# Performance work log

Measured on AMD Instinct MI355X. Metric: run time of the kernel, lower is better.

## Reference

```python
import jax, jax.numpy as jnp
import numpy as np

N_HEADS = 16
ROPE_BASE = 10000.0


def setup_inputs() -> dict:
    key = jax.random.key(0)
    k1, k2, k3 = jax.random.split(key, 3)
    B, L, D = 2, 2048, 2048
    x = jax.random.normal(k1, (B, L, D), dtype=jnp.float32)
    w_qkv = jax.random.normal(k2, (D, 3 * D), dtype=jnp.float32) * (1.0 / np.sqrt(D))
    w_out = jax.random.normal(k3, (D, D), dtype=jnp.float32) * (1.0 / np.sqrt(D))
    return {"x": x, "w_qkv": w_qkv, "w_out": w_out}


def _rope_cos_sin(L, head_dim, dtype):
    # inv_freq over even dims, freqs duplicated across both halves (HF convention)
    inv_freq = 1.0 / (ROPE_BASE ** (jnp.arange(0, head_dim, 2, dtype=jnp.float32) / head_dim))
    freqs = jnp.arange(L, dtype=jnp.float32)[:, None] * inv_freq[None, :]  # [L, hd/2]
    emb = jnp.concatenate([freqs, freqs], axis=-1)  # [L, hd]
    return jnp.cos(emb).astype(dtype), jnp.sin(emb).astype(dtype)


def _rotate_half(t):
    h = t.shape[-1] // 2
    return jnp.concatenate([-t[..., h:], t[..., :h]], axis=-1)


def reference(x, w_qkv, w_out):
    B, L, D = x.shape
    H = N_HEADS
    hd = D // H
    qkv = x @ w_qkv  # [B, L, 3D]
    q, k, v = jnp.split(qkv, 3, axis=-1)

    def heads(t):  # [B, L, D] -> [B, H, L, hd]
        return t.reshape(B, L, H, hd).transpose(0, 2, 1, 3)

    q, k, v = heads(q), heads(k), heads(v)
    cos, sin = _rope_cos_sin(L, hd, x.dtype)  # [L, hd] broadcast over B,H
    q = q * cos + _rotate_half(q) * sin
    k = k * cos + _rotate_half(k) * sin
    # SDPA, no mask, no dropout (eval), not causal
    scale = 1.0 / np.sqrt(hd)
    scores = jnp.einsum('bhld,bhsd->bhls', q, k) * scale
    attn = jax.nn.softmax(scores, axis=-1)
    y = jnp.einsum('bhls,bhsd->bhld', attn, v)  # [B, H, L, hd]
    y = y.transpose(0, 2, 1, 3).reshape(B, L, D)
    return y @ w_out
```

## Files before the change

kernel.cpp:

```cpp
#include <hip/hip_runtime.h>

typedef __attribute__((ext_vector_type(8))) short bf16x8;
typedef __attribute__((ext_vector_type(8))) unsigned short u16x8;
typedef __attribute__((ext_vector_type(4))) float f32x4;
typedef __attribute__((ext_vector_type(16))) float f32x16;
typedef __attribute__((ext_vector_type(4))) unsigned short u16x4;
typedef __attribute__((ext_vector_type(4))) unsigned int u32x4;
typedef unsigned int u32;

#define BB 2
#define LL 2048
#define DD 2048
#define HH 16
#define HDIM 128
#define MM 4096
#define NQKV 6144

__device__ __forceinline__ unsigned short f2bf(float f) {
    unsigned int u = __builtin_bit_cast(unsigned int, f);
    u += 0x7FFFu + ((u >> 16) & 1u);
    return (unsigned short)(u >> 16);
}
__device__ __forceinline__ float bf2f(unsigned short h) {
    unsigned int u = ((unsigned int)h) << 16;
    return __builtin_bit_cast(float, u);
}

__device__ __forceinline__ void gload16(const unsigned short* g, unsigned short* l) {
    __builtin_amdgcn_global_load_lds((const __attribute__((address_space(1))) void*)g,
                                     (__attribute__((address_space(3))) void*)l, 16, 0, 0);
}

__device__ __forceinline__ u32 cvtpk(float lo, float hi) {
    u32 r;
    asm("v_cvt_pk_bf16_f32 %0, %1, %2" : "=v"(r) : "v"(lo), "v"(hi));
    return r;
}
__device__ __forceinline__ void plswap(u32& a, u32& b) {
    asm("v_permlane32_swap_b32 %0, %1" : "+v"(a), "+v"(b));
}

__global__ __launch_bounds__(256) void k_prep(const float* __restrict__ x, unsigned short* __restrict__ xb,
                                              const float* __restrict__ wqkv, unsigned short* __restrict__ wqkvT,
                                              const float* __restrict__ wout, unsigned short* __restrict__ woutT,
                                              float* __restrict__ ct, float* __restrict__ st) {
    __shared__ unsigned short t[64][72];
    int bid = blockIdx.x;
    int tid = threadIdx.x;
    if (bid < 8192) {
        int i = bid * 256 + tid;
        float4 v = reinterpret_cast<const float4*>(x)[i];
        u16x4 o;
        o[0] = f2bf(v.x); o[1] = f2bf(v.y); o[2] = f2bf(v.z); o[3] = f2bf(v.w);
        reinterpret_cast<u16x4*>(xb)[i] = o;
        return;
    }
    if (bid >= 12288) {
        int idx = (bid - 12288) * 256 + tid;
        int pos = idx >> 6, d = idx & 63;
        float freq = __expf(-(float)d * (9.210340371976184f / 64.0f));
        float ang = (float)pos * freq;
        ct[idx] = cosf(ang);
        st[idx] = sinf(ang);
        return;
    }
    const float* in; unsigned short* out; int K, N, n0, k0;
    if (bid < 11264) {
        int r = bid - 8192;
        in = wqkv; out = wqkvT; K = DD; N = NQKV;
        n0 = (r % 96) * 64; k0 = (r / 96) * 64;
    } else {
        int r = bid - 11264;
        in = wout; out = woutT; K = DD; N = DD;
        n0 = (r & 31) * 64; k0 = (r >> 5) * 64;
    }
    int tr = tid >> 4, tc = tid & 15;
    #pragma unroll
    for (int i = 0; i < 4; ++i) {
        int k = i * 16 + tr;
        float4 v = *reinterpret_cast<const float4*>(in + (size_t)(k0 + k) * N + n0 + tc * 4);
        t[tc * 4 + 0][k] = f2bf(v.x);
        t[tc * 4 + 1][k] = f2bf(v.y);
        t[tc * 4 + 2][k] = f2bf(v.z);
        t[tc * 4 + 3][k] = f2bf(v.w);
    }
    __syncthreads();
    #pragma unroll
    for (int i = 0; i < 4; ++i) {
        int n = i * 16 + tr;
        u16x4 o = *reinterpret_cast<u16x4*>(&t[n][tc * 4]);
        *reinterpret_cast<u16x4*>(out + (size_t)(n0 + n) * K + k0 + tc * 4) = o;
    }
}

__global__ __launch_bounds__(256) void k_transV(const unsigned short* __restrict__ in,
                                                unsigned short* __restrict__ out) {
    __shared__ unsigned short t[64][68];
    int l0 = blockIdx.x * 64, d0 = blockIdx.y * 64;
    int bh = blockIdx.z;
    const unsigned short* ib = in + (size_t)bh * LL * HDIM;
    unsigned short* ob = out + (size_t)bh * HDIM * LL;
    int tid = threadIdx.x;
    int tr = tid >> 4, tc = tid & 15;
    #pragma unroll
    for (int i = 0; i < 4; ++i) {
        int l = i * 16 + tr;
        u16x4 v = *reinterpret_cast<const u16x4*>(ib + (size_t)(l0 + l) * HDIM + d0 + tc * 4);
        t[tc * 4 + 0][l] = v[0];
        t[tc * 4 + 1][l] = v[1];
        t[tc * 4 + 2][l] = v[2];
        t[tc * 4 + 3][l] = v[3];
    }
    __syncthreads();
    #pragma unroll
    for (int i = 0; i < 4; ++i) {
        int d = i * 16 + tr;
        u16x4 o = *reinterpret_cast<u16x4*>(&t[d][tc * 4]);
        *reinterpret_cast<u16x4*>(ob + (size_t)(d0 + d) * LL + l0 + tc * 4) = o;
    }
}

__global__ __launch_bounds__(256) void k_rope_apply(unsigned short* __restrict__ Q,
                                                    unsigned short* __restrict__ K,
                                                    const float* __restrict__ ct,
                                                    const float* __restrict__ st) {
    int idx = blockIdx.x * 256 + threadIdx.x;
    int d = idx & 63;
    int pos = (idx >> 6) & (LL - 1);
    int bh = idx >> 17;
    size_t base = ((size_t)bh * LL + pos) * HDIM;
    float c = ct[pos * 64 + d], s = st[pos * 64 + d];
    float q0 = bf2f(Q[base + d]), q1 = bf2f(Q[base + d + 64]);
    Q[base + d]      = f2bf(q0 * c - q1 * s);
    Q[base + d + 64] = f2bf(q1 * c + q0 * s);
    float k0 = bf2f(K[base + d]), k1 = bf2f(K[base + d + 64]);
    K[base + d]      = f2bf(k0 * c - k1 * s);
    K[base + d + 64] = f2bf(k1 * c + k0 * s);
}

__global__ __launch_bounds__(512, 2) void k_gemm384(const unsigned short* __restrict__ A,
                                                    const unsigned short* __restrict__ Bt,
                                                    unsigned short* __restrict__ outQ,
                                                    unsigned short* __restrict__ outK,
                                                    unsigned short* __restrict__ outV) {
    __shared__ unsigned short sm[3 * 20480];
    const int Kn = DD;
    const int tid = threadIdx.x;
    const int lane = tid & 63, w = tid >> 6;
    const int wm = w >> 2, wn = w & 3;
    const int lrow = lane & 15, lgrp = lane >> 4;
    const int NT = Kn / 32;

    int orig = blockIdx.x;
    int tau = (orig & 7) * 32 + (orig >> 3);
    const int m0 = (tau & 15) * 256, n0 = (tau >> 4) * 384;

    const int srow = lane >> 2, scol = lane & 3;
    const int scolg = ((scol ^ ((srow >> 1) & 3)) * 8);
    const int fcol  = ((lgrp ^ ((lrow >> 1) & 3)) * 8);

    f32x4 acc[8][6] = {};

    auto stageA = [&](int t, int r) {
        unsigned short* dst = sm + (t % 3) * 20480 + (r * 128 + w * 16) * 32;
        gload16(A + (size_t)(m0 + r * 128 + w * 16 + srow) * Kn + t * 32 + scolg, dst);
    };
    auto stageB = [&](int t, int r) {
        unsigned short* dst = sm + (t % 3) * 20480 + 8192 + (r * 128 + w * 16) * 32;
        gload16(Bt + (size_t)(n0 + r * 128 + w * 16 + srow) * Kn + t * 32 + scolg, dst);
    };

    auto body = [&](int t, bool doStage) {
        unsigned short* bufA = sm + (t % 3) * 20480;
        unsigned short* bufB = bufA + 8192;
        bf16x8 af[8], bfr[2];
        #pragma unroll
        for (int f = 0; f < 8; ++f)
            af[f] = *reinterpret_cast<const bf16x8*>(bufA + (wm * 128 + f * 16 + lrow) * 32 + fcol);
        bfr[0] = *reinterpret_cast<const bf16x8*>(bufB + (wn * 96 + 0 * 16 + lrow) * 32 + fcol);
        bfr[1] = *reinterpret_cast<const bf16x8*>(bufB + (wn * 96 + 1 * 16 + lrow) * 32 + fcol);
        if (doStage) { stageA(t + 2, 0); stageA(t + 2, 1); }
        __builtin_amdgcn_s_barrier();
        __builtin_amdgcn_s_setprio(1);
        #pragma unroll
        for (int fm = 0; fm < 8; ++fm)
            #pragma unroll
            for (int j = 0; j < 2; ++j)
                acc[fm][j] = __builtin_amdgcn_mfma_f32_16x16x32_bf16(af[fm], bfr[j], acc[fm][j], 0, 0, 0);
        __builtin_amdgcn_s_setprio(0);
        bfr[0] = *reinterpret_cast<const bf16x8*>(bufB + (wn * 96 + 2 * 16 + lrow) * 32 + fcol);
        bfr[1] = *reinterpret_cast<const bf16x8*>(bufB + (wn * 96 + 3 * 16 + lrow) * 32 + fcol);
        if (doStage) { stageB(t + 2, 0); stageB(t + 2, 1); }
        __builtin_amdgcn_s_barrier();
        __builtin_amdgcn_s_setprio(1);
        #pragma unroll
        for (int fm = 0; fm < 8; ++fm)
            #pragma unroll
            for (int j = 0; j < 2; ++j)
                acc[fm][2 + j] = __builtin_amdgcn_mfma_f32_16x16x32_bf16(af[fm], bfr[j], acc[fm][2 + j], 0, 0, 0);
        __builtin_amdgcn_s_setprio(0);
        bfr[0] = *reinterpret_cast<const bf16x8*>(bufB + (wn * 96 + 4 * 16 + lrow) * 32 + fcol);
        bfr[1] = *reinterpret_cast<const bf16x8*>(bufB + (wn * 96 + 5 * 16 + lrow) * 32 + fcol);
        if (doStage) { stageB(t + 2, 2); }
        __builtin_amdgcn_s_barrier();
        __builtin_amdgcn_s_setprio(1);
        #pragma unroll
        for (int fm = 0; fm < 8; ++fm)
            #pragma unroll
            for (int j = 0; j < 2; ++j)
                acc[fm][4 + j] = __builtin_amdgcn_mfma_f32_16x16x32_bf16(af[fm], bfr[j], acc[fm][4 + j], 0, 0, 0);
        __builtin_amdgcn_s_setprio(0);
    };

    stageA(0, 0); stageA(0, 1); stageB(0, 0); stageB(0, 1); stageB(0, 2);
    stageA(1, 0); stageA(1, 1); stageB(1, 0); stageB(1, 1); stageB(1, 2);
    asm volatile("s_waitcnt vmcnt(5)" ::: "memory");
    __builtin_amdgcn_s_barrier();

    for (int t = 0; t < NT - 2; ++t) {
        body(t, true);
        asm volatile("s_waitcnt vmcnt(5)" ::: "memory");
        __builtin_amdgcn_s_barrier();
    }
    body(NT - 2, false);
    asm volatile("s_waitcnt vmcnt(0)" ::: "memory");
    __builtin_amdgcn_s_barrier();
    body(NT - 1, false);

    #pragma unroll
    for (int fm = 0; fm < 8; ++fm) {
        int mrow = m0 + wm * 128 + fm * 16 + lgrp * 4;
        #pragma unroll
        for (int fn = 0; fn < 6; ++fn) {
            int ncol = n0 + wn * 96 + fn * 16 + lrow;
            int which = ncol >> 11;
            int rr = ncol & (DD - 1);
            int h = rr >> 7, d = rr & (HDIM - 1);
            unsigned short* dst = (which == 0) ? outQ : ((which == 1) ? outK : outV);
            #pragma unroll
            for (int i = 0; i < 4; ++i) {
                int m = mrow + i;
                int b = m >> 11, pos = m & (LL - 1);
                dst[((size_t)(b * HH + h) * LL + pos) * HDIM + d] = f2bf(acc[fm][fn][i]);
            }
        }
    }
}

__global__ __launch_bounds__(512) void k_gemm2x(const unsigned short* __restrict__ A,
                                                const unsigned short* __restrict__ Bt,
                                                float* __restrict__ outC) {
    __shared__ unsigned short sm[4 * 12288];
    const int Kn = DD, Nn = DD;
    const int tid = threadIdx.x;
    const int lane = tid & 63, w = tid >> 6;
    const int wm = w >> 1, wn = w & 1;
    const int lrow = lane & 15, lgrp = lane >> 4;
    const int NT = Kn / 32;

    int orig = blockIdx.x;
    int tau = (orig & 7) * 32 + (orig >> 3);
    const int m0 = (tau & 15) * 256, n0 = (tau >> 4) * 128;

    const int srow = lane >> 2, scol = lane & 3;
    const int scolg = ((scol ^ ((srow >> 1) & 3)) * 8);
    const int fcol  = ((lgrp ^ ((lrow >> 1) & 3)) * 8);

    f32x4 acc[4][4] = {};

    auto stage = [&](int t) {
        const int kb = t * 32;
        unsigned short* buf = sm + (t & 3) * 12288;
        gload16(A  + (size_t)(m0 + w * 16 + srow) * Kn + kb + scolg,        buf + w * 512);
        gload16(A  + (size_t)(m0 + 128 + w * 16 + srow) * Kn + kb + scolg,  buf + 4096 + w * 512);
        gload16(Bt + (size_t)(n0 + w * 16 + srow) * Kn + kb + scolg,        buf + 8192 + w * 512);
    };

    auto tile_body = [&](int t, bool do_stage) {
        unsigned short* buf = sm + (t & 3) * 12288;
        bf16x8 af[4], bfr[4];
        #pragma unroll
        for (int f = 0; f < 4; ++f)
            af[f] = *reinterpret_cast<const bf16x8*>(buf + (wm * 64 + f * 16 + lrow) * 32 + fcol);
        #pragma unroll
        for (int f = 0; f < 4; ++f)
            bfr[f] = *reinterpret_cast<const bf16x8*>(buf + 8192 + (wn * 64 + f * 16 + lrow) * 32 + fcol);
        if (do_stage) stage(t + 3);
        __builtin_amdgcn_s_barrier();
        __builtin_amdgcn_s_setprio(1);
        #pragma unroll
        for (int fm = 0; fm < 4; ++fm)
            #pragma unroll
            for (int fn = 0; fn < 4; ++fn)
                acc[fm][fn] = __builtin_amdgcn_mfma_f32_16x16x32_bf16(af[fm], bfr[fn], acc[fm][fn], 0, 0, 0);
        __builtin_amdgcn_s_setprio(0);
    };

    stage(0); stage(1); stage(2);
    asm volatile("s_waitcnt vmcnt(6)" ::: "memory");
    __builtin_amdgcn_s_barrier();

    for (int t = 0; t < NT - 3; ++t) {
        tile_body(t, true);
        asm volatile("s_waitcnt vmcnt(6)" ::: "memory");
        __builtin_amdgcn_s_barrier();
    }
    tile_body(NT - 3, false);
    asm volatile("s_waitcnt vmcnt(3)" ::: "memory");
    __builtin_amdgcn_s_barrier();
    tile_body(NT - 2, false);
    asm volatile("s_waitcnt vmcnt(0)" ::: "memory");
    __builtin_amdgcn_s_barrier();
    tile_body(NT - 1, false);

    #pragma unroll
    for (int fm = 0; fm < 4; ++fm) {
        int mrow = m0 + wm * 64 + fm * 16 + lgrp * 4;
        #pragma unroll
        for (int fn = 0; fn < 4; ++fn) {
            int ncol = n0 + wn * 64 + fn * 16 + lrow;
            #pragma unroll
            for (int i = 0; i < 4; ++i)
                outC[(size_t)(mrow + i) * (size_t)Nn + ncol] = acc[fm][fn][i];
        }
    }
}

__global__ __launch_bounds__(256, 2) void k_attn(const unsigned short* __restrict__ Q,
                                                 const unsigned short* __restrict__ K,
                                                 const unsigned short* __restrict__ Vt,
                                                 unsigned short* __restrict__ Y) {
    __shared__ unsigned short Kl[2][64][136];
    __shared__ unsigned short VTl[2][128][72];
    int tid = threadIdx.x;
    int lane = tid & 63, w = tid >> 6;
    int l31 = lane & 31, hl = lane >> 5;
    int orig = blockIdx.x;
    int id = (orig & 7) * 64 + (orig >> 3);
    int bh = id >> 4, qt = id & 15;
    int b = bh >> 4, hh = bh & 15;
    const unsigned short* Qb = Q  + (size_t)bh * LL * HDIM;
    const unsigned short* Kb = K  + (size_t)bh * LL * HDIM;
    const unsigned short* Vb = Vt + (size_t)bh * HDIM * LL;
    int q0 = qt * 128 + w * 32;

    bf16x8 qf[8];
    #pragma unroll
    for (int kk = 0; kk < 8; ++kk)
        qf[kk] = *reinterpret_cast<const bf16x8*>(
            Qb + (size_t)(q0 + l31) * HDIM + kk * 16 + hl * 8);

    f32x16 accO[4] = {};
    float accLs = 0.0f;
    const float scale = 0.08838834764831845f;

    u16x8 kr[4], vr[4];
    auto sload = [&](int kt) {
        #pragma unroll
        for (int i = 0; i < 4; ++i) {
            int c = i * 256 + tid;
            kr[i] = *reinterpret_cast<const u16x8*>(Kb + (size_t)(kt * 64 + (c >> 4)) * HDIM + (c & 15) * 8);
            vr[i] = *reinterpret_cast<const u16x8*>(Vb + (size_t)(c >> 3) * LL + kt * 64 + (c & 7) * 8);
        }
    };
    auto swrite = [&](int buf) {
        #pragma unroll
        for (int i = 0; i < 4; ++i) {
            int c = i * 256 + tid;
            *reinterpret_cast<u16x8*>(&Kl[buf][c >> 4][(c & 15) * 8]) = kr[i];
            *reinterpret_cast<u16x8*>(&VTl[buf][c >> 3][(c & 7) * 8]) = vr[i];
        }
    };

    sload(0);
    swrite(0);
    __syncthreads();

    for (int kt = 0; kt < LL / 64; ++kt) {
        int cb = kt & 1;
        if (kt + 1 < LL / 64) sload(kt + 1);

        f32x16 s[2] = {};
        __builtin_amdgcn_s_setprio(1);
        #pragma unroll
        for (int kk = 0; kk < 8; ++kk) {
            bf16x8 kf0 = *reinterpret_cast<const bf16x8*>(&Kl[cb][l31][kk * 16 + hl * 8]);
            bf16x8 kf1 = *reinterpret_cast<const bf16x8*>(&Kl[cb][32 + l31][kk * 16 + hl * 8]);
            s[0] = __builtin_amdgcn_mfma_f32_32x32x16_bf16(kf0, qf[kk], s[0], 0, 0, 0);
            s[1] = __builtin_amdgcn_mfma_f32_32x32x16_bf16(kf1, qf[kk], s[1], 0, 0, 0);
        }
        __builtin_amdgcn_s_setprio(0);

        bf16x8 pa[2][2];
        #pragma unroll
        for (int kn = 0; kn < 2; ++kn) {
            float p[16];
            #pragma unroll
            for (int r = 0; r < 16; ++r) {
                p[r] = __expf(s[kn][r] * scale);
                accLs += p[r];
            }
            #pragma unroll
            for (int ksub = 0; ksub < 2; ++ksub) {
                const int bse = ksub * 8;
                u32 a0 = cvtpk(p[bse + 0], p[bse + 1]);
                u32 a1 = cvtpk(p[bse + 2], p[bse + 3]);
                u32 b0 = cvtpk(p[bse + 4], p[bse + 5]);
                u32 b1 = cvtpk(p[bse + 6], p[bse + 7]);
                plswap(a0, b0);
                plswap(a1, b1);
                u32x4 fw; fw[0] = a0; fw[1] = a1; fw[2] = b0; fw[3] = b1;
                pa[kn][ksub] = __builtin_bit_cast(bf16x8, fw);
            }
        }

        __builtin_amdgcn_s_setprio(1);
        #pragma unroll
        for (int kn = 0; kn < 2; ++kn)
            #pragma unroll
            for (int ksub = 0; ksub < 2; ++ksub) {
                #pragma unroll
                for (int dn = 0; dn < 4; ++dn) {
                    bf16x8 vf = *reinterpret_cast<const bf16x8*>(
                        &VTl[cb][dn * 32 + l31][kn * 32 + ksub * 16 + hl * 8]);
                    accO[dn] = __builtin_amdgcn_mfma_f32_32x32x16_bf16(pa[kn][ksub], vf, accO[dn], 0, 0, 0);
                }
            }
        __builtin_amdgcn_s_setprio(0);

        if (kt + 1 < LL / 64) swrite(cb ^ 1);
        __syncthreads();
    }

    float tot = accLs + __shfl_xor(accLs, 32);

    #pragma unroll
    for (int r = 0; r < 16; ++r) {
        int qrow = (r & 3) + 8 * (r >> 2) + 4 * hl;
        float l = __shfl(tot, qrow);
        float inv = 1.0f / l;
        int pos = q0 + qrow;
        #pragma unroll
        for (int dn = 0; dn < 4; ++dn) {
            int d = dn * 32 + l31;
            Y[((size_t)b * LL + pos) * DD + hh * HDIM + d] = f2bf(accO[dn][r] * inv);
        }
    }
}

extern "C" void kernel_launch(void* const* d_in, const int* in_sizes, int n_in,
                              void* d_out, int out_size, void* d_ws, size_t ws_size,
                              hipStream_t stream) {
    const float* x     = (const float*)d_in[0];
    const float* wqkv  = (const float*)d_in[1];
    const float* wout  = (const float*)d_in[2];
    float* out = (float*)d_out;

    char* ws = (char*)d_ws;
    size_t off = 0;
    auto take = [&](size_t bytes) { char* p = ws + off; off += (bytes + 255) & ~(size_t)255; return p; };
    unsigned short* xb    = (unsigned short*)take((size_t)MM * DD * 2);
    unsigned short* wqkvT = (unsigned short*)take((size_t)DD * NQKV * 2);
    unsigned short* woutT = (unsigned short*)take((size_t)DD * DD * 2);
    unsigned short* Qb    = (unsigned short*)take((size_t)BB * HH * LL * HDIM * 2);
    unsigned short* Kb    = (unsigned short*)take((size_t)BB * HH * LL * HDIM * 2);
    unsigned short* Vb    = (unsigned short*)take((size_t)BB * HH * LL * HDIM * 2);
    unsigned short* Yb    = (unsigned short*)take((size_t)MM * DD * 2);
    float* ct             = (float*)take((size_t)LL * 64 * 4);
    float* st             = (float*)take((size_t)LL * 64 * 4);
    if (off > ws_size) return;
    unsigned short* VtB = xb;

    k_prep<<<12800, 256, 0, stream>>>(x, xb, wqkv, wqkvT, wout, woutT, ct, st);

    k_gemm384<<<256, 512, 0, stream>>>(xb, wqkvT, Qb, Kb, Vb);
    k_transV<<<dim3(LL / 64, HDIM / 64, BB * HH), 256, 0, stream>>>(Vb, VtB);
    k_rope_apply<<<(BB * HH * LL * 64) / 256, 256, 0, stream>>>(Qb, Kb, ct, st);
    k_attn<<<BB * HH * (LL / 128), 256, 0, stream>>>(Qb, Kb, VtB, Yb);
    k_gemm2x<<<256, 512, 0, stream>>>(Yb, woutT, out);
}
```

Baseline: 248.4 us.

## Fuse V transpose with K RoPE and apply Q RoPE inside attention

```diff
diff --git a/kernel.cpp b/kernel.cpp
--- a/kernel.cpp
+++ b/kernel.cpp
@@ -93,49 +93,56 @@
     }
 }
 
-__global__ __launch_bounds__(256) void k_transV(const unsigned short* __restrict__ in,
-                                                unsigned short* __restrict__ out) {
+__global__ __launch_bounds__(256) void k_tvrope(const unsigned short* __restrict__ V,
+                                                unsigned short* __restrict__ Vt,
+                                                unsigned short* __restrict__ K,
+                                                const float* __restrict__ ct,
+                                                const float* __restrict__ st) {
     __shared__ unsigned short t[64][68];
-    int l0 = blockIdx.x * 64, d0 = blockIdx.y * 64;
-    int bh = blockIdx.z;
-    const unsigned short* ib = in + (size_t)bh * LL * HDIM;
-    unsigned short* ob = out + (size_t)bh * HDIM * LL;
+    int bid = blockIdx.x;
     int tid = threadIdx.x;
-    int tr = tid >> 4, tc = tid & 15;
-    #pragma unroll
-    for (int i = 0; i < 4; ++i) {
-        int l = i * 16 + tr;
-        u16x4 v = *reinterpret_cast<const u16x4*>(ib + (size_t)(l0 + l) * HDIM + d0 + tc * 4);
-        t[tc * 4 + 0][l] = v[0];
-        t[tc * 4 + 1][l] = v[1];
-        t[tc * 4 + 2][l] = v[2];
-        t[tc * 4 + 3][l] = v[3];
-    }
-    __syncthreads();
-    #pragma unroll
-    for (int i = 0; i < 4; ++i) {
-        int d = i * 16 + tr;
-        u16x4 o = *reinterpret_cast<u16x4*>(&t[d][tc * 4]);
-        *reinterpret_cast<u16x4*>(ob + (size_t)(d0 + d) * LL + l0 + tc * 4) = o;
-    }
-}
-
-__global__ __launch_bounds__(256) void k_rope_apply(unsigned short* __restrict__ Q,
-                                                    unsigned short* __restrict__ K,
-                                                    const float* __restrict__ ct,
-                                                    const float* __restrict__ st) {
-    int idx = blockIdx.x * 256 + threadIdx.x;
-    int d = idx & 63;
-    int pos = (idx >> 6) & (LL - 1);
-    int bh = idx >> 17;
-    size_t base = ((size_t)bh * LL + pos) * HDIM;
-    float c = ct[pos * 64 + d], s = st[pos * 64 + d];
-    float q0 = bf2f(Q[base + d]), q1 = bf2f(Q[base + d + 64]);
-    Q[base + d]      = f2bf(q0 * c - q1 * s);
-    Q[base + d + 64] = f2bf(q1 * c + q0 * s);
-    float k0 = bf2f(K[base + d]), k1 = bf2f(K[base + d + 64]);
-    K[base + d]      = f2bf(k0 * c - k1 * s);
-    K[base + d + 64] = f2bf(k1 * c + k0 * s);
+    if (bid < 2048) {
+        int bh = bid >> 6;
+        int l0 = ((bid >> 1) & 31) * 64;
+        int d0 = (bid & 1) * 64;
+        const unsigned short* ib = V + (size_t)bh * LL * HDIM;
+        unsigned short* ob = Vt + (size_t)bh * HDIM * LL;
+        int tr = tid >> 4, tc = tid & 15;
+        #pragma unroll
+        for (int i = 0; i < 4; ++i) {
+            int l = i * 16 + tr;
+            u16x4 v = *reinterpret_cast<const u16x4*>(ib + (size_t)(l0 + l) * HDIM + d0 + tc * 4);
+            t[tc * 4 + 0][l] = v[0];
+            t[tc * 4 + 1][l] = v[1];
+            t[tc * 4 + 2][l] = v[2];
+            t[tc * 4 + 3][l] = v[3];
+        }
+        __syncthreads();
+        #pragma unroll
+        for (int i = 0; i < 4; ++i) {
+            int d = i * 16 + tr;
+            u16x4 o = *reinterpret_cast<u16x4*>(&t[d][tc * 4]);
+            *reinterpret_cast<u16x4*>(ob + (size_t)(d0 + d) * LL + l0 + tc * 4) = o;
+        }
+    } else {
+        int idx = (bid - 2048) * 256 + tid;
+        int d0 = (idx & 7) * 8;
+        int pos = (idx >> 3) & (LL - 1);
+        int bh = idx >> 14;
+        size_t base = ((size_t)bh * LL + pos) * HDIM;
+        u16x8 k0 = *reinterpret_cast<const u16x8*>(K + base + d0);
+        u16x8 k1 = *reinterpret_cast<const u16x8*>(K + base + 64 + d0);
+        u16x8 o0, o1;
+        #pragma unroll
+        for (int j = 0; j < 8; ++j) {
+            float c = ct[pos * 64 + d0 + j], s = st[pos * 64 + d0 + j];
+            float a = bf2f(k0[j]), b = bf2f(k1[j]);
+            o0[j] = f2bf(a * c - b * s);
+            o1[j] = f2bf(b * c + a * s);
+        }
+        *reinterpret_cast<u16x8*>(K + base + d0) = o0;
+        *reinterpret_cast<u16x8*>(K + base + 64 + d0) = o1;
+    }
 }
 
 __global__ __launch_bounds__(512, 2) void k_gemm384(const unsigned short* __restrict__ A,
@@ -188,6 +195,7 @@
             for (int j = 0; j < 2; ++j)
                 acc[fm][j] = __builtin_amdgcn_mfma_f32_16x16x32_bf16(af[fm], bfr[j], acc[fm][j], 0, 0, 0);
         __builtin_amdgcn_s_setprio(0);
+        __builtin_amdgcn_s_barrier();
         bfr[0] = *reinterpret_cast<const bf16x8*>(bufB + (wn * 96 + 2 * 16 + lrow) * 32 + fcol);
         bfr[1] = *reinterpret_cast<const bf16x8*>(bufB + (wn * 96 + 3 * 16 + lrow) * 32 + fcol);
         if (doStage) { stageB(t + 2, 0); stageB(t + 2, 1); }
@@ -199,6 +207,7 @@
             for (int j = 0; j < 2; ++j)
                 acc[fm][2 + j] = __builtin_amdgcn_mfma_f32_16x16x32_bf16(af[fm], bfr[j], acc[fm][2 + j], 0, 0, 0);
         __builtin_amdgcn_s_setprio(0);
+        __builtin_amdgcn_s_barrier();
         bfr[0] = *reinterpret_cast<const bf16x8*>(bufB + (wn * 96 + 4 * 16 + lrow) * 32 + fcol);
         bfr[1] = *reinterpret_cast<const bf16x8*>(bufB + (wn * 96 + 5 * 16 + lrow) * 32 + fcol);
         if (doStage) { stageB(t + 2, 2); }
@@ -329,7 +338,9 @@
 __global__ __launch_bounds__(256, 2) void k_attn(const unsigned short* __restrict__ Q,
                                                  const unsigned short* __restrict__ K,
                                                  const unsigned short* __restrict__ Vt,
-                                                 unsigned short* __restrict__ Y) {
+                                                 unsigned short* __restrict__ Y,
+                                                 const float* __restrict__ ct,
+                                                 const float* __restrict__ st) {
     __shared__ unsigned short Kl[2][64][136];
     __shared__ unsigned short VTl[2][128][72];
     int tid = threadIdx.x;
@@ -349,6 +360,26 @@
     for (int kk = 0; kk < 8; ++kk)
         qf[kk] = *reinterpret_cast<const bf16x8*>(
             Qb + (size_t)(q0 + l31) * HDIM + kk * 16 + hl * 8);
+    {
+        int pos = q0 + l31;
+        #pragma unroll
+        for (int kk = 0; kk < 4; ++kk) {
+            int d0 = kk * 16 + hl * 8;
+            float4 c0 = *reinterpret_cast<const float4*>(ct + pos * 64 + d0);
+            float4 c1 = *reinterpret_cast<const float4*>(ct + pos * 64 + d0 + 4);
+            float4 s0 = *reinterpret_cast<const float4*>(st + pos * 64 + d0);
+            float4 s1 = *reinterpret_cast<const float4*>(st + pos * 64 + d0 + 4);
+            float cs[8] = {c0.x, c0.y, c0.z, c0.w, c1.x, c1.y, c1.z, c1.w};
+            float sn[8] = {s0.x, s0.y, s0.z, s0.w, s1.x, s1.y, s1.z, s1.w};
+            #pragma unroll
+            for (int j = 0; j < 8; ++j) {
+                float a = bf2f((unsigned short)qf[kk][j]);
+                float bb2 = bf2f((unsigned short)qf[kk + 4][j]);
+                qf[kk][j]     = (short)f2bf(a * cs[j] - bb2 * sn[j]);
+                qf[kk + 4][j] = (short)f2bf(bb2 * cs[j] + a * sn[j]);
+            }
+        }
+    }
 
     f32x16 accO[4] = {};
     float accLs = 0.0f;
@@ -474,8 +505,7 @@
     k_prep<<<12800, 256, 0, stream>>>(x, xb, wqkv, wqkvT, wout, woutT, ct, st);
 
     k_gemm384<<<256, 512, 0, stream>>>(xb, wqkvT, Qb, Kb, Vb);
-    k_transV<<<dim3(LL / 64, HDIM / 64, BB * HH), 256, 0, stream>>>(Vb, VtB);
-    k_rope_apply<<<(BB * HH * LL * 64) / 256, 256, 0, stream>>>(Qb, Kb, ct, st);
-    k_attn<<<BB * HH * (LL / 128), 256, 0, stream>>>(Qb, Kb, VtB, Yb);
+    k_tvrope<<<4096, 256, 0, stream>>>(Vb, VtB, Kb, ct, st);
+    k_attn<<<BB * HH * (LL / 128), 256, 0, stream>>>(Qb, Kb, VtB, Yb, ct, st);
     k_gemm2x<<<256, 512, 0, stream>>>(Yb, woutT, out);
 }
```

After: 246.0 us. About the same (-1.0%).
